# Kernel optimization log

Measured on AMD Instinct MI355X. Metric: run time of the kernel, lower is better.

Reference implementation:

```python
import jax, jax.numpy as jnp
import numpy as np

N, E, IN_DIM, H, OUT, MAPD = 20000, 640000, 24, 128, 24, 512
SLOPE = 0.01  # torch F.leaky_relu default


def setup_inputs() -> dict:
    key = jax.random.key(0)
    ks = jax.random.split(key, 20)
    g = lambda i, shape, s: jax.random.normal(ks[i], shape, jnp.float32) * s
    inp = {
        "feats": g(0, (N, IN_DIM), 1.0),
        "e_w": jax.random.uniform(ks[1], (E, 1), dtype=jnp.float32),
        "maps_embedding": g(2, (N, MAPD), 1.0),
        "snorm_n": jnp.ones((N, 1), jnp.float32),
        "src": jax.random.randint(ks[3], (E,), 0, N),
        "dst": jax.random.randint(ks[4], (E,), 0, N),
        "W_eh": g(5, (H, IN_DIM), (2.0 / IN_DIM) ** 0.5), "b_eh": jnp.zeros((H,), jnp.float32),
        "W_ee": g(6, (H, 1), 1.0), "b_ee": jnp.zeros((H,), jnp.float32),
        "W_cat": g(7, (H, H + MAPD), (2.0 / (H + MAPD)) ** 0.5), "b_cat": jnp.zeros((H,), jnp.float32),
        "Ws1": g(8, (H, H), (2.0 / H) ** 0.5), "Wf1": g(9, (H, H), (2.0 / H) ** 0.5),
        "a1": g(10, (2 * H,), (2.0 / (2 * H)) ** 0.5),
        "Ws2": g(11, (H, H), (2.0 / H) ** 0.5), "Wf2": g(12, (H, H), (2.0 / H) ** 0.5),
        "a2": g(13, (2 * H,), (2.0 / (2 * H)) ** 0.5),
        "W_out": g(14, (OUT, H), (2.0 / H) ** 0.5), "b_out": jnp.zeros((OUT,), jnp.float32),
    }
    return inp


def gat_layer(h, src, dst, Ws, Wf, a):
    # My_GATLayer with (as constructed in My_GAT) relu=False, att_ew=False, dropouts=0.
    h_in = h
    h_s = h @ Ws.T                         # [N,H] self transform
    z = h @ Wf.T                           # [N,H] message transform
    # attention score = leaky_relu(a^T [z_src, z_dst]) computed via per-node halves
    s_src = z @ a[:H]                      # [N]
    s_dst = z @ a[H:]                      # [N]
    e = jax.nn.leaky_relu(s_src[src] + s_dst[dst], SLOPE)          # [E]
    # numerically stable segment softmax over incoming edges grouped by dst
    m = jax.ops.segment_max(e, dst, num_segments=N)
    m = jnp.where(jnp.isfinite(m), m, 0.0)
    ex = jnp.exp(e - m[dst])
    denom = jax.ops.segment_sum(ex, dst, num_segments=N)
    alpha = ex / jnp.maximum(denom[dst], 1e-16)                    # [E]
    agg = jax.ops.segment_sum(alpha[:, None] * z[src], dst, num_segments=N)  # [N,H]
    indeg = jax.ops.segment_sum(jnp.ones_like(e), dst, num_segments=N)
    # DGL update_all leaves zero-in-degree nodes at their prior ndata['h'] (= h_in)
    h_node = jnp.where(indeg[:, None] > 0, h_s + agg, h_in)
    return h_in + h_node                   # residual connection; relu disabled (positional-arg bug)


def reference(feats, e_w, maps_embedding, snorm_n, src, dst,
              W_eh, b_eh, W_ee, b_ee, W_cat, b_cat,
              Ws1, Wf1, a1, Ws2, Wf2, a2, W_out, b_out):
    feats = feats.reshape(feats.shape[0], -1)
    h = feats @ W_eh.T + b_eh                                  # embedding_h
    _e = e_w @ W_ee.T + b_ee                                   # edge embedding (stored on g.edata['w'], unused since att_ew binds to attn_drop)
    h = jnp.concatenate([maps_embedding, h], axis=-1) @ W_cat.T + b_cat
    h = jax.nn.relu(h)
    h = gat_layer(h, src, dst, Ws1, Wf1, a1)
    h = gat_layer(h, src, dst, Ws2, Wf2, a2)
    return h @ W_out.T + b_out
```

## Files before the change

kernel.cpp:

```cpp
#include <hip/hip_runtime.h>

#define HBLK 128
#define EPB 4096

typedef __attribute__((ext_vector_type(8))) short s8v;
typedef __attribute__((ext_vector_type(4))) float f32x4;
typedef __attribute__((ext_vector_type(8))) _Float16 h8f;

__device__ inline void split2(float x, short& h, short& l) {
    unsigned hb = __float_as_uint(x) & 0xFFFF0000u;
    float hf = __uint_as_float(hb);
    float lf = x - hf;
    h = (short)(hb >> 16);
    l = (short)(__float_as_uint(lf) >> 16);
}

__device__ inline void split8(const float4& a0, const float4& a1, s8v& ah, s8v& al) {
    float vv[8];
    *(float4*)&vv[0] = a0;
    *(float4*)&vv[4] = a1;
#pragma unroll
    for (int e = 0; e < 8; ++e) {
        short hh, ll;
        split2(vv[e], hh, ll);
        ah[e] = hh;
        al[e] = ll;
    }
}


__global__ void bin_hist(const int* __restrict__ dst, int* __restrict__ histT,
                         int E, int NB1) {
    __shared__ int h[256];
    const int t = threadIdx.x, blk = blockIdx.x;
    h[t] = 0;
    __syncthreads();
    const int e0 = blk * EPB;
    const int e1 = min(E, e0 + EPB);
    for (int e = e0 + t; e < e1; e += 256)
        atomicAdd(&h[dst[e] >> 7], 1);
    __syncthreads();
    histT[t * NB1 + blk] = h[t];
}

__global__ void scan1(const int* __restrict__ counts, int* __restrict__ offs,
                      int* __restrict__ bsums, int n) {
    __shared__ int lds[256];
    const int t = threadIdx.x;
    const int i = blockIdx.x * 256 + t;
    const int v = (i < n) ? counts[i] : 0;
    lds[t] = v;
    __syncthreads();
    for (int off = 1; off < 256; off <<= 1) {
        int add = (t >= off) ? lds[t - off] : 0;
        __syncthreads();
        lds[t] += add;
        __syncthreads();
    }
    if (i < n) offs[i] = lds[t] - v;
    if (t == 255) bsums[blockIdx.x] = lds[255];
}

__global__ void scan2(int* __restrict__ bsums, int nb) {
    __shared__ int lds[256];
    const int t = threadIdx.x;
    const int v = (t < nb) ? bsums[t] : 0;
    lds[t] = v;
    __syncthreads();
    for (int off = 1; off < 256; off <<= 1) {
        int add = (t >= off) ? lds[t - off] : 0;
        __syncthreads();
        lds[t] += add;
        __syncthreads();
    }
    if (t < nb) bsums[t] = lds[t] - v;
}

__global__ void scan3g(int* __restrict__ data, const int* __restrict__ bsums, int n) {
    const int i = blockIdx.x * 256 + threadIdx.x;
    if (i < n) data[i] += bsums[blockIdx.x];
}

__global__ void bin_scatter(const int* __restrict__ src, const int* __restrict__ dst,
                            const int* __restrict__ histT, int2* __restrict__ ebuf,
                            int E, int NB1) {
    __shared__ int cur[256];
    const int t = threadIdx.x, blk = blockIdx.x;
    cur[t] = histT[t * NB1 + blk];
    __syncthreads();
    const int e0 = blk * EPB;
    const int e1 = min(E, e0 + EPB);
    for (int e = e0 + t; e < e1; e += 256) {
        const int d = dst[e];
        const int p = atomicAdd(&cur[d >> 7], 1);
        ebuf[p] = make_int2(src[e], d);
    }
}

__global__ void bucket_sort(const int2* __restrict__ ebuf, const int* __restrict__ histT,
                            int* __restrict__ offs, int* __restrict__ srcs,
                            int N, int E, int NB1) {
    __shared__ int cnt[256];
    __shared__ int cur[256];
    const int t = threadIdx.x, b = blockIdx.x;
    const int ebase = histT[b * NB1];
    const int eend = (b + 1 < 256) ? histT[(b + 1) * NB1] : E;
    cnt[t] = 0;
    __syncthreads();
    for (int e = ebase + t; e < eend; e += 256)
        atomicAdd(&cnt[ebuf[e].y & 127], 1);
    __syncthreads();
    const int own = cnt[t];
    for (int off = 1; off < 256; off <<= 1) {
        int add = (t >= off) ? cnt[t - off] : 0;
        __syncthreads();
        cnt[t] += add;
        __syncthreads();
    }
    const int excl = cnt[t] - own;
    cur[t] = ebase + excl;
    const int node = (b << 7) + t;
    if (t < 128 && node < N) offs[node] = ebase + excl;
    if (b == 0 && t == 0) offs[N] = E;
    __syncthreads();
    for (int e = ebase + t; e < eend; e += 256) {
        const int2 ed = ebuf[e];
        const int p = atomicAdd(&cur[ed.y & 127], 1);
        srcs[p] = ed.x;
    }
}

__global__ void make_wcomb(const float* __restrict__ Wcat, int ldw, int mapd,
                           const float* __restrict__ Weh, int indim,
                           const float* __restrict__ beh, const float* __restrict__ bcat,
                           float* __restrict__ Wcomb, float* __restrict__ bcomb) {
    const int i = blockIdx.x * 256 + threadIdx.x;
    const int total = HBLK * indim;
    if (i < total) {
        const int c = i / indim, k = i % indim;
        const float* wc = Wcat + (long)c * ldw + mapd;
        float s = 0.f;
        for (int j = 0; j < HBLK; ++j) s += wc[j] * Weh[j * indim + k];
        Wcomb[(long)c * indim + k] = s;
    } else if (i < total + HBLK) {
        const int c = i - total;
        const float* wc = Wcat + (long)c * ldw + mapd;
        float s = bcat[c];
        for (int j = 0; j < HBLK; ++j) s += wc[j] * beh[j];
        bcomb[c] = s;
    }
}

__global__ void split_w_pack(const float* __restrict__ W, int ldw, int kin, int cin,
                             short* __restrict__ dh, short* __restrict__ dl,
                             int C, int K) {
    long i = (long)blockIdx.x * 256 + threadIdx.x;
    if (i >= (long)C * K) return;
    int c = (int)(i / K), k = (int)(i % K);
    float x = (k < kin && c < cin) ? W[(long)c * ldw + k] : 0.f;
    short h, l;
    split2(x, h, l);
    int nj = C >> 4;
    int j = c >> 4, l16 = c & 15;
    int chunk = k >> 5, quad = (k >> 3) & 3, t = k & 7;
    long off = (((long)(chunk * nj + j) * 64) + quad * 16 + l16) * 8 + t;
    dh[off] = h;
    dl[off] = l;
}

__global__ void pack_wcat(const float* __restrict__ Wcat, int ldw, int mapd,
                          const float* __restrict__ Wcomb, int indim,
                          short* __restrict__ dh, short* __restrict__ dl, int K) {
    long i = (long)blockIdx.x * 256 + threadIdx.x;
    if (i >= (long)HBLK * K) return;
    int c = (int)(i / K), k = (int)(i % K);
    float x = 0.f;
    if (k < mapd) x = Wcat[(long)c * ldw + k];
    else if (k < mapd + indim) x = Wcomb[(long)c * indim + (k - mapd)];
    short h, l;
    split2(x, h, l);
    int j = c >> 4, l16 = c & 15;
    int chunk = k >> 5, quad = (k >> 3) & 3, t = k & 7;
    long off = (((long)(chunk * 8 + j) * 64) + quad * 16 + l16) * 8 + t;
    dh[off] = h;
    dl[off] = l;
}

__global__ void split_w_pack4(const float* __restrict__ W0, const float* __restrict__ W1,
                              const float* __restrict__ W2, const float* __restrict__ W3,
                              short* __restrict__ dh, short* __restrict__ dl) {
    const float* Ws[4] = {W0, W1, W2, W3};
    const int m = blockIdx.y;
    long i = (long)blockIdx.x * 256 + threadIdx.x;
    int c = (int)(i >> 7), k = (int)(i & 127);
    float x = Ws[m][c * HBLK + k];
    short h, l;
    split2(x, h, l);
    int j = c >> 4, l16 = c & 15;
    int chunk = k >> 5, quad = (k >> 3) & 3, t = k & 7;
    long off = (long)m * 16384 + (((long)(chunk * 8 + j) * 64) + quad * 16 + l16) * 8 + t;
    dh[off] = h;
    dl[off] = l;
}

__global__ __launch_bounds__(256, 2) void gemm_bigk(
    const float* __restrict__ A1, int lda1, int K1,
    const float* __restrict__ A2, int lda2, int Kin,
    int K,
    const short* __restrict__ Wh, const short* __restrict__ Wl,
    const float* __restrict__ bias,
    float* __restrict__ Cf, int M)
{
    __shared__ short lds_h[2][4096];
    __shared__ short lds_l[2][4096];
    const int tid = threadIdx.x;
    const int wv = tid >> 6;
    const int lane = tid & 63;
    const int l16 = lane & 15;
    const int quad = lane >> 4;
    const int m0 = blockIdx.x * 64 + wv * 16;
    int ra = m0 + l16;
    if (ra >= M) ra = M - 1;
    const long r1 = (long)ra * lda1;
    const long r2 = (long)ra * lda2;
    const int NC = K >> 5;

    f32x4 acc[8];
#pragma unroll
    for (int j = 0; j < 8; ++j) acc[j] = (f32x4){0.f, 0.f, 0.f, 0.f};

#define LOAD_A(d0, d1, kb)                                      \
    {                                                           \
        const int col0 = (kb) + quad * 8;                       \
        if (col0 < K1) {                                        \
            const float* ap = A1 + r1 + col0;                   \
            d0 = *(const float4*)ap;                            \
            d1 = *(const float4*)(ap + 4);                      \
        } else if (col0 < Kin) {                                \
            const float* ap = A2 + r2 + (col0 - K1);            \
            d0 = *(const float4*)ap;                            \
            d1 = *(const float4*)(ap + 4);                      \
        } else {                                                \
            d0 = make_float4(0.f, 0.f, 0.f, 0.f);               \
            d1 = make_float4(0.f, 0.f, 0.f, 0.f);               \
        }                                                       \
    }
#define LOAD_W(c)                                               \
    {                                                           \
        const int4* gh = (const int4*)(Wh + (long)(c) * 4096);  \
        const int4* gl = (const int4*)(Wl + (long)(c) * 4096);  \
        wh0 = gh[tid * 2]; wh1 = gh[tid * 2 + 1];               \
        wl0 = gl[tid * 2]; wl1 = gl[tid * 2 + 1];               \
    }
#define WRITE_W(b)                                              \
    {                                                           \
        int4* bh = (int4*)lds_h[b];                             \
        int4* bl = (int4*)lds_l[b];                             \
        bh[tid * 2] = wh0; bh[tid * 2 + 1] = wh1;               \
        bl[tid * 2] = wl0; bl[tid * 2 + 1] = wl1;               \
    }

    int4 wh0, wh1, wl0, wl1;
    LOAD_W(0)
    WRITE_W(0)
    LOAD_W(1)
    float4 a0c, a1c, a0n, a1n;
    float4 a0p = make_float4(0.f, 0.f, 0.f, 0.f);
    float4 a1p = make_float4(0.f, 0.f, 0.f, 0.f);
    LOAD_A(a0c, a1c, 0)
    LOAD_A(a0n, a1n, 32)
    asm volatile("s_waitcnt lgkmcnt(0)" ::: "memory");
    __builtin_amdgcn_s_barrier();
    asm volatile("" ::: "memory");

    for (int c = 0; c < NC; ++c) {
        const int nb = c & 1;
        if (c + 2 < NC) {
            LOAD_A(a0p, a1p, (c + 2) * 32)
        }
        s8v ah, al;
        split8(a0c, a1c, ah, al);
#pragma unroll
        for (int j = 0; j < 8; ++j) {
            const s8v whf = *(const s8v*)&lds_h[nb][(j * 64 + lane) * 8];
            const s8v wlf = *(const s8v*)&lds_l[nb][(j * 64 + lane) * 8];
            acc[j] = __builtin_amdgcn_mfma_f32_16x16x32_bf16(ah, whf, acc[j], 0, 0, 0);
            acc[j] = __builtin_amdgcn_mfma_f32_16x16x32_bf16(ah, wlf, acc[j], 0, 0, 0);
            acc[j] = __builtin_amdgcn_mfma_f32_16x16x32_bf16(al, whf, acc[j], 0, 0, 0);
        }
        if (c + 1 < NC) {
            WRITE_W(nb ^ 1)
            if (c + 2 < NC) LOAD_W(c + 2)
            asm volatile("s_waitcnt lgkmcnt(0)" ::: "memory");
            __builtin_amdgcn_s_barrier();
            asm volatile("" ::: "memory");
        }
        a0c = a0n; a1c = a1n; a0n = a0p; a1n = a1p;
    }
#undef LOAD_A
#undef LOAD_W
#undef WRITE_W

#pragma unroll
    for (int r = 0; r < 4; ++r) {
        const int gr = m0 + quad * 4 + r;
        if (gr >= M) continue;
#pragma unroll
        for (int j = 0; j < 8; ++j) {
            const int col = j * 16 + l16;
            float v = acc[j][r] + bias[col];
            Cf[(long)gr * HBLK + col] = fmaxf(v, 0.f);
        }
    }
}

__global__ __launch_bounds__(256, 2) void gemm_smallk(
    const float* __restrict__ A,
    const short* __restrict__ W1h, const short* __restrict__ W1l,
    const short* __restrict__ W2h, const short* __restrict__ W2l,
    float* __restrict__ C1f, _Float16* __restrict__ Czh,
    const float* __restrict__ avec,
    float* __restrict__ sOut, float* __restrict__ dOut, int M)
{
    __shared__ short lh[16384];
    __shared__ short ll[16384];
    const short* __restrict__ Wh = blockIdx.y ? W2h : W1h;
    const short* __restrict__ Wl = blockIdx.y ? W2l : W1l;
    float* __restrict__ Cf = blockIdx.y ? nullptr : C1f;
    _Float16* __restrict__ Ch16 = blockIdx.y ? Czh : nullptr;
    const float* __restrict__ av = blockIdx.y ? avec : nullptr;
    const int tid = threadIdx.x;
    const int wv = tid >> 6;
    const int lane = tid & 63;
    const int l16 = lane & 15;
    const int quad = lane >> 4;
    const int m0 = blockIdx.x * 64 + wv * 16;
    int ra = m0 + l16;
    if (ra >= M) ra = M - 1;
    const float* arow = A + (long)ra * HBLK + quad * 8;

    {
        const int4* gh = (const int4*)Wh;
        const int4* gl = (const int4*)Wl;
        int4* bh = (int4*)lh;
        int4* bl = (int4*)ll;
#pragma unroll
        for (int i = 0; i < 8; ++i) {
            bh[i * 256 + tid] = gh[i * 256 + tid];
            bl[i * 256 + tid] = gl[i * 256 + tid];
        }
    }
    float4 aw0[4], aw1[4];
#pragma unroll
    for (int c = 0; c < 4; ++c) {
        aw0[c] = *(const float4*)(arow + c * 32);
        aw1[c] = *(const float4*)(arow + c * 32 + 4);
    }
    f32x4 acc[8];
#pragma unroll
    for (int j = 0; j < 8; ++j) acc[j] = (f32x4){0.f, 0.f, 0.f, 0.f};
    __syncthreads();

#pragma unroll
    for (int c = 0; c < 4; ++c) {
        s8v ah, al;
        split8(aw0[c], aw1[c], ah, al);
#pragma unroll
        for (int j = 0; j < 8; ++j) {
            const s8v whf = *(const s8v*)&lh[((c * 8 + j) * 64 + lane) * 8];
            const s8v wlf = *(const s8v*)&ll[((c * 8 + j) * 64 + lane) * 8];
            acc[j] = __builtin_amdgcn_mfma_f32_16x16x32_bf16(ah, whf, acc[j], 0, 0, 0);
            acc[j] = __builtin_amdgcn_mfma_f32_16x16x32_bf16(ah, wlf, acc[j], 0, 0, 0);
            acc[j] = __builtin_amdgcn_mfma_f32_16x16x32_bf16(al, whf, acc[j], 0, 0, 0);
        }
    }

#pragma unroll
    for (int r = 0; r < 4; ++r) {
        const int gr = m0 + quad * 4 + r;
        if (gr >= M) continue;
#pragma unroll
        for (int j = 0; j < 8; ++j) {
            const int col = j * 16 + l16;
            const float v = acc[j][r];
            if (Cf) Cf[(long)gr * HBLK + col] = v;
            if (Ch16) Ch16[(long)gr * HBLK + col] = (_Float16)v;
        }
    }

    if (av) {
        float av0[8], av1[8];
#pragma unroll
        for (int j = 0; j < 8; ++j) {
            av0[j] = av[j * 16 + l16];
            av1[j] = av[128 + j * 16 + l16];
        }
#pragma unroll
        for (int r = 0; r < 4; ++r) {
            float ssp = 0.f, sdp = 0.f;
#pragma unroll
            for (int j = 0; j < 8; ++j) {
                const float v = acc[j][r];
                ssp += v * av0[j];
                sdp += v * av1[j];
            }
#pragma unroll
            for (int off = 1; off < 16; off <<= 1) {
                ssp += __shfl_xor(ssp, off);
                sdp += __shfl_xor(sdp, off);
            }
            const int gr = m0 + quad * 4 + r;
            if (l16 == 0 && gr < M) {
                sOut[gr] = ssp;
                dOut[gr] = sdp;
            }
        }
    }
}

__global__ __launch_bounds__(256) void gemm_out(
    const float* __restrict__ A,
    const short* __restrict__ Wh, const short* __restrict__ Wl,
    const float* __restrict__ bias, float* __restrict__ out,
    int M, int OUTD)
{
    __shared__ short lh[4096], ll[4096];
    const int tid = threadIdx.x;
    {
        const int4* gh = (const int4*)Wh;
        const int4* gl = (const int4*)Wl;
        int4* bh = (int4*)lh;
        int4* bl = (int4*)ll;
        bh[tid * 2] = gh[tid * 2];
        bh[tid * 2 + 1] = gh[tid * 2 + 1];
        bl[tid * 2] = gl[tid * 2];
        bl[tid * 2 + 1] = gl[tid * 2 + 1];
    }
    const int wv = tid >> 6;
    const int lane = tid & 63;
    const int l16 = lane & 15;
    const int quad = lane >> 4;
    const int m0 = blockIdx.x * 64 + wv * 16;
    int ra = m0 + l16;
    if (ra >= M) ra = M - 1;
    const float* arow = A + (long)ra * HBLK + quad * 8;

    f32x4 acc[2];
    acc[0] = (f32x4){0.f, 0.f, 0.f, 0.f};
    acc[1] = (f32x4){0.f, 0.f, 0.f, 0.f};
    __syncthreads();

#pragma unroll
    for (int c = 0; c < 4; ++c) {
        const float4 a0 = *(const float4*)(arow + c * 32);
        const float4 a1 = *(const float4*)(arow + c * 32 + 4);
        s8v ah, al;
        split8(a0, a1, ah, al);
#pragma unroll
        for (int j = 0; j < 2; ++j) {
            const s8v whf = *(const s8v*)&lh[((c * 2 + j) * 64 + lane) * 8];
            const s8v wlf = *(const s8v*)&ll[((c * 2 + j) * 64 + lane) * 8];
            acc[j] = __builtin_amdgcn_mfma_f32_16x16x32_bf16(ah, whf, acc[j], 0, 0, 0);
            acc[j] = __builtin_amdgcn_mfma_f32_16x16x32_bf16(ah, wlf, acc[j], 0, 0, 0);
            acc[j] = __builtin_amdgcn_mfma_f32_16x16x32_bf16(al, whf, acc[j], 0, 0, 0);
        }
    }

#pragma unroll
    for (int r = 0; r < 4; ++r) {
        const int gr = m0 + quad * 4 + r;
        if (gr >= M) continue;
#pragma unroll
        for (int j = 0; j < 2; ++j) {
            const int col = j * 16 + l16;
            if (col < OUTD)
                out[(long)gr * OUTD + col] = acc[j][r] + bias[col];
        }
    }
}

__global__ void gat_gather(const float* __restrict__ h_in, const float* __restrict__ hs,
                           const _Float16* __restrict__ zh,
                           const float* __restrict__ s_src, const float* __restrict__ s_dst,
                           const int* __restrict__ offs, const int* __restrict__ srcs,
                           float* __restrict__ h_out, int N) {
    const int wave = threadIdx.x >> 6;
    const int lane = threadIdx.x & 63;
    const int n = blockIdx.x * 4 + wave;
    if (n >= N) return;
    const int g = lane >> 4, l = lane & 15;
    const int beg = offs[n], end = offs[n + 1];

    float acc[8] = {};
    if (end > beg) {
        const float sd = s_dst[n];
        float m = -INFINITY, s = 0.f;
        for (int i = beg + lane; i < end; i += 64) {
            float e = sd + s_src[srcs[i]];
            e = e > 0.f ? e : 0.01f * e;
            float nm = fmaxf(m, e);
            s = s * __expf(m - nm) + __expf(e - nm);
            m = nm;
        }
#pragma unroll
        for (int off = 32; off > 0; off >>= 1) {
            float m2 = __shfl_down(m, off);
            float s2 = __shfl_down(s, off);
            if (m2 > m) {
                float t = m; m = m2; m2 = t;
                float ts = s; s = s2; s2 = ts;
            }
            s = (m == -INFINITY) ? 0.f : s + s2 * __expf(m2 - m);
        }
        m = __shfl(m, 0);
        s = __shfl(s, 0);
        const float inv = 1.f / fmaxf(s, 1e-16f);

        int i = beg + g;
        for (; i + 4 < end; i += 8) {
            const int s0 = srcs[i];
            const int s1 = srcs[i + 4];
            float e0 = sd + s_src[s0];
            float e1 = sd + s_src[s1];
            e0 = e0 > 0.f ? e0 : 0.01f * e0;
            e1 = e1 > 0.f ? e1 : 0.01f * e1;
            const float w0 = __expf(e0 - m) * inv;
            const float w1 = __expf(e1 - m) * inv;
            const h8f z0 = *(const h8f*)(zh + (long)s0 * HBLK + 8 * l);
            const h8f z1 = *(const h8f*)(zh + (long)s1 * HBLK + 8 * l);
#pragma unroll
            for (int e = 0; e < 8; ++e)
                acc[e] += w0 * (float)z0[e] + w1 * (float)z1[e];
        }
        if (i < end) {
            const int s0 = srcs[i];
            float e0 = sd + s_src[s0];
            e0 = e0 > 0.f ? e0 : 0.01f * e0;
            const float w0 = __expf(e0 - m) * inv;
            const h8f z0 = *(const h8f*)(zh + (long)s0 * HBLK + 8 * l);
#pragma unroll
            for (int e = 0; e < 8; ++e)
                acc[e] += w0 * (float)z0[e];
        }
#pragma unroll
        for (int e = 0; e < 8; ++e) {
            acc[e] += __shfl_down(acc[e], 32);
            acc[e] += __shfl_down(acc[e], 16);
        }
    }

    if (g == 0) {
        const long base = (long)n * HBLK + 8 * l;
        const float4 hi0 = *(const float4*)(h_in + base);
        const float4 hi1 = *(const float4*)(h_in + base + 4);
        float o[8];
        if (end > beg) {
            const float4 hv0 = *(const float4*)(hs + base);
            const float4 hv1 = *(const float4*)(hs + base + 4);
            const float* hip = (const float*)&hi0;
            const float* hvp = (const float*)&hv0;
#pragma unroll
            for (int e = 0; e < 4; ++e) o[e] = hip[e] + hvp[e] + acc[e];
            const float* hip1 = (const float*)&hi1;
            const float* hvp1 = (const float*)&hv1;
#pragma unroll
            for (int e = 0; e < 4; ++e) o[4 + e] = hip1[e] + hvp1[e] + acc[4 + e];
        } else {
            const float* hip = (const float*)&hi0;
            const float* hip1 = (const float*)&hi1;
#pragma unroll
            for (int e = 0; e < 4; ++e) o[e] = 2.f * hip[e];
#pragma unroll
            for (int e = 0; e < 4; ++e) o[4 + e] = 2.f * hip1[e];
        }
        *(float4*)(h_out + base) = *(float4*)&o[0];
        *(float4*)(h_out + base + 4) = *(float4*)&o[4];
    }
}

extern "C" void kernel_launch(void* const* d_in, const int* in_sizes, int n_in,
                              void* d_out, int out_size, void* d_ws, size_t ws_size,
                              hipStream_t stream) {
    const float* feats = (const float*)d_in[0];
    const float* maps  = (const float*)d_in[2];
    const int* src = (const int*)d_in[4];
    const int* dst = (const int*)d_in[5];
    const float* W_eh  = (const float*)d_in[6];
    const float* b_eh  = (const float*)d_in[7];
    const float* W_cat = (const float*)d_in[10];
    const float* b_cat = (const float*)d_in[11];
    const float* Ws1 = (const float*)d_in[12];
    const float* Wf1 = (const float*)d_in[13];
    const float* a1  = (const float*)d_in[14];
    const float* Ws2 = (const float*)d_in[15];
    const float* Wf2 = (const float*)d_in[16];
    const float* a2  = (const float*)d_in[17];
    const float* W_out = (const float*)d_in[18];
    const float* b_out = (const float*)d_in[19];

    const int N = in_sizes[3];
    const int E = in_sizes[4];
    const int IN_DIM = in_sizes[0] / N;
    const int MAPD = in_sizes[2] / N;
    const int OUTD = in_sizes[19];
    const int KCAT = MAPD + HBLK;
    const int KC = (MAPD + IN_DIM + 31) & ~31;

    char* p = (char*)d_ws;
    const size_t NH = (size_t)N * HBLK;
    float* hin  = (float*)p;  p += NH * 4;
    float* hs   = (float*)p;  p += NH * 4;
    float* hout = (float*)p;  p += NH * 4;
    _Float16* zh = (_Float16*)p; p += NH * 2;
    float* ssrc = (float*)p;  p += (size_t)N * 4;
    float* sdst = (float*)p;  p += (size_t)N * 4;
    int* offs   = (int*)p;    p += (size_t)(N + 1) * 4;
    int* srcs   = (int*)p;    p += (size_t)E * 4;
    int* bsums  = (int*)p;    p += 256 * 4;
    int* histT  = (int*)p;    p += (size_t)256 * 256 * 4;
    float* Wcomb = (float*)p; p += (size_t)HBLK * IN_DIM * 4;
    float* bcomb = (float*)p; p += (size_t)HBLK * 4;
    p = (char*)(((uintptr_t)p + 15) & ~(uintptr_t)15);
    int2* ebuf = (int2*)p;    p += (size_t)E * 8;
    short* Wcat_h = (short*)p; p += (size_t)HBLK * KC * 2;
    short* Wcat_l = (short*)p; p += (size_t)HBLK * KC * 2;
    short* Wout_h = (short*)p; p += (size_t)32 * HBLK * 2;
    short* Wout_l = (short*)p; p += (size_t)32 * HBLK * 2;
    short* Wly_h = (short*)p;  p += (size_t)4 * HBLK * HBLK * 2;
    short* Wly_l = (short*)p;  p += (size_t)4 * HBLK * HBLK * 2;

    const int NB1 = (E + EPB - 1) / EPB;
    const int NBUCK = (N + 127) >> 7;
    const int nHist = 256 * NB1;
    bin_hist<<<NB1, 256, 0, stream>>>(dst, histT, E, NB1);
    scan1<<<NB1, 256, 0, stream>>>(histT, histT, bsums, nHist);
    scan2<<<1, 256, 0, stream>>>(bsums, NB1);
    scan3g<<<NB1, 256, 0, stream>>>(histT, bsums, nHist);
    bin_scatter<<<NB1, 256, 0, stream>>>(src, dst, histT, ebuf, E, NB1);
    bucket_sort<<<NBUCK, 256, 0, stream>>>(ebuf, histT, offs, srcs, N, E, NB1);

    make_wcomb<<<(HBLK * IN_DIM + HBLK + 255) / 256, 256, 0, stream>>>(
        W_cat, KCAT, MAPD, W_eh, IN_DIM, b_eh, b_cat, Wcomb, bcomb);
    pack_wcat<<<(HBLK * KC + 255) / 256, 256, 0, stream>>>(
        W_cat, KCAT, MAPD, Wcomb, IN_DIM, Wcat_h, Wcat_l, KC);
    split_w_pack4<<<dim3(64, 4), 256, 0, stream>>>(Ws1, Wf1, Ws2, Wf2, Wly_h, Wly_l);
    split_w_pack<<<(32 * HBLK + 255) / 256, 256, 0, stream>>>(
        W_out, HBLK, HBLK, OUTD, Wout_h, Wout_l, 32, HBLK);

    const int gGrid = (N + 63) / 64;
    const int n4 = (N + 3) / 4;

    gemm_bigk<<<gGrid, 256, 0, stream>>>(
        maps, MAPD, MAPD, feats, IN_DIM, MAPD + IN_DIM, KC,
        Wcat_h, Wcat_l, bcomb, hin, N);

    gemm_smallk<<<dim3(gGrid, 2), 256, 0, stream>>>(
        hin, Wly_h, Wly_l, Wly_h + 16384, Wly_l + 16384,
        hs, zh, a1, ssrc, sdst, N);
    gat_gather<<<n4, 256, 0, stream>>>(hin, hs, zh, ssrc, sdst, offs, srcs, hout, N);

    gemm_smallk<<<dim3(gGrid, 2), 256, 0, stream>>>(
        hout, Wly_h + 32768, Wly_l + 32768, Wly_h + 49152, Wly_l + 49152,
        hs, zh, a2, ssrc, sdst, N);
    gat_gather<<<n4, 256, 0, stream>>>(hout, hs, zh, ssrc, sdst, offs, srcs, hin, N);

    gemm_out<<<gGrid, 256, 0, stream>>>(hin, Wout_h, Wout_l, b_out, (float*)d_out, N, OUTD);
}
```

Baseline: 274.1 us.

## Fold scan fixup and weight packing into fewer launches, deepen prefetch and unroll gather

Removes the scan3g kernel by adding block sums inline in bin_scatter and bucket_sort. Merges make_wcomb into pack_wcat and folds the W_out packing into split_w_packA, cutting three launches in total. Separately, gemm_bigk now prefetches weights and A one chunk further ahead, and the GAT gather loop processes four edges per iteration instead of two. The deeper prefetch and wider unroll raise register pressure, and each pack_wcat thread does a 128-long dot product for the combined columns.

```diff
diff --git a/kernel.cpp b/kernel.cpp
--- a/kernel.cpp
+++ b/kernel.cpp
@@ -76,17 +76,13 @@
     if (t < nb) bsums[t] = lds[t] - v;
 }
 
-__global__ void scan3g(int* __restrict__ data, const int* __restrict__ bsums, int n) {
-    const int i = blockIdx.x * 256 + threadIdx.x;
-    if (i < n) data[i] += bsums[blockIdx.x];
-}
-
 __global__ void bin_scatter(const int* __restrict__ src, const int* __restrict__ dst,
-                            const int* __restrict__ histT, int2* __restrict__ ebuf,
-                            int E, int NB1) {
+                            const int* __restrict__ histT, const int* __restrict__ bsums,
+                            int2* __restrict__ ebuf, int E, int NB1) {
     __shared__ int cur[256];
     const int t = threadIdx.x, blk = blockIdx.x;
-    cur[t] = histT[t * NB1 + blk];
+    const int li = t * NB1 + blk;
+    cur[t] = histT[li] + bsums[li >> 8];
     __syncthreads();
     const int e0 = blk * EPB;
     const int e1 = min(E, e0 + EPB);
@@ -98,13 +94,19 @@
 }
 
 __global__ void bucket_sort(const int2* __restrict__ ebuf, const int* __restrict__ histT,
+                            const int* __restrict__ bsums,
                             int* __restrict__ offs, int* __restrict__ srcs,
                             int N, int E, int NB1) {
     __shared__ int cnt[256];
     __shared__ int cur[256];
     const int t = threadIdx.x, b = blockIdx.x;
-    const int ebase = histT[b * NB1];
-    const int eend = (b + 1 < 256) ? histT[(b + 1) * NB1] : E;
+    const int li0 = b * NB1;
+    const int ebase = histT[li0] + bsums[li0 >> 8];
+    int eend = E;
+    if (b + 1 < 256) {
+        const int li1 = (b + 1) * NB1;
+        eend = histT[li1] + bsums[li1 >> 8];
+    }
     cnt[t] = 0;
     __syncthreads();
     for (int e = ebase + t; e < eend; e += 256)
@@ -130,20 +132,34 @@
     }
 }
 
-__global__ void make_wcomb(const float* __restrict__ Wcat, int ldw, int mapd,
-                           const float* __restrict__ Weh, int indim,
-                           const float* __restrict__ beh, const float* __restrict__ bcat,
-                           float* __restrict__ Wcomb, float* __restrict__ bcomb) {
-    const int i = blockIdx.x * 256 + threadIdx.x;
-    const int total = HBLK * indim;
+__global__ void pack_wcat(const float* __restrict__ Wcat, int ldw, int mapd,
+                          const float* __restrict__ Weh, int indim,
+                          const float* __restrict__ beh, const float* __restrict__ bcat,
+                          short* __restrict__ dh, short* __restrict__ dl,
+                          float* __restrict__ bcomb, int K) {
+    const long i = (long)blockIdx.x * 256 + threadIdx.x;
+    const long total = (long)HBLK * K;
     if (i < total) {
-        const int c = i / indim, k = i % indim;
-        const float* wc = Wcat + (long)c * ldw + mapd;
-        float s = 0.f;
-        for (int j = 0; j < HBLK; ++j) s += wc[j] * Weh[j * indim + k];
-        Wcomb[(long)c * indim + k] = s;
+        const int c = (int)(i / K), k = (int)(i % K);
+        float x = 0.f;
+        if (k < mapd) {
+            x = Wcat[(long)c * ldw + k];
+        } else if (k < mapd + indim) {
+            const float* wc = Wcat + (long)c * ldw + mapd;
+            const int kk = k - mapd;
+            float s = 0.f;
+            for (int j = 0; j < HBLK; ++j) s += wc[j] * Weh[j * indim + kk];
+            x = s;
+        }
+        short h, l;
+        split2(x, h, l);
+        const int j = c >> 4, l16 = c & 15;
+        const int chunk = k >> 5, quad = (k >> 3) & 3, t = k & 7;
+        const long off = (((long)(chunk * 8 + j) * 64) + quad * 16 + l16) * 8 + t;
+        dh[off] = h;
+        dl[off] = l;
     } else if (i < total + HBLK) {
-        const int c = i - total;
+        const int c = (int)(i - total);
         const float* wc = Wcat + (long)c * ldw + mapd;
         float s = bcat[c];
         for (int j = 0; j < HBLK; ++j) s += wc[j] * beh[j];
@@ -151,56 +167,36 @@
     }
 }
 
-__global__ void split_w_pack(const float* __restrict__ W, int ldw, int kin, int cin,
-                             short* __restrict__ dh, short* __restrict__ dl,
-                             int C, int K) {
-    long i = (long)blockIdx.x * 256 + threadIdx.x;
-    if (i >= (long)C * K) return;
-    int c = (int)(i / K), k = (int)(i % K);
-    float x = (k < kin && c < cin) ? W[(long)c * ldw + k] : 0.f;
-    short h, l;
-    split2(x, h, l);
-    int nj = C >> 4;
-    int j = c >> 4, l16 = c & 15;
-    int chunk = k >> 5, quad = (k >> 3) & 3, t = k & 7;
-    long off = (((long)(chunk * nj + j) * 64) + quad * 16 + l16) * 8 + t;
-    dh[off] = h;
-    dl[off] = l;
-}
-
-__global__ void pack_wcat(const float* __restrict__ Wcat, int ldw, int mapd,
-                          const float* __restrict__ Wcomb, int indim,
-                          short* __restrict__ dh, short* __restrict__ dl, int K) {
-    long i = (long)blockIdx.x * 256 + threadIdx.x;
-    if (i >= (long)HBLK * K) return;
-    int c = (int)(i / K), k = (int)(i % K);
-    float x = 0.f;
-    if (k < mapd) x = Wcat[(long)c * ldw + k];
-    else if (k < mapd + indim) x = Wcomb[(long)c * indim + (k - mapd)];
-    short h, l;
-    split2(x, h, l);
-    int j = c >> 4, l16 = c & 15;
-    int chunk = k >> 5, quad = (k >> 3) & 3, t = k & 7;
-    long off = (((long)(chunk * 8 + j) * 64) + quad * 16 + l16) * 8 + t;
-    dh[off] = h;
-    dl[off] = l;
-}
-
-__global__ void split_w_pack4(const float* __restrict__ W0, const float* __restrict__ W1,
+__global__ void split_w_packA(const float* __restrict__ W0, const float* __restrict__ W1,
                               const float* __restrict__ W2, const float* __restrict__ W3,
-                              short* __restrict__ dh, short* __restrict__ dl) {
-    const float* Ws[4] = {W0, W1, W2, W3};
+                              const float* __restrict__ Wout, int outd,
+                              short* __restrict__ dh, short* __restrict__ dl,
+                              short* __restrict__ doh, short* __restrict__ dol) {
     const int m = blockIdx.y;
-    long i = (long)blockIdx.x * 256 + threadIdx.x;
-    int c = (int)(i >> 7), k = (int)(i & 127);
-    float x = Ws[m][c * HBLK + k];
-    short h, l;
-    split2(x, h, l);
-    int j = c >> 4, l16 = c & 15;
-    int chunk = k >> 5, quad = (k >> 3) & 3, t = k & 7;
-    long off = (long)m * 16384 + (((long)(chunk * 8 + j) * 64) + quad * 16 + l16) * 8 + t;
-    dh[off] = h;
-    dl[off] = l;
+    const long i = (long)blockIdx.x * 256 + threadIdx.x;
+    if (m < 4) {
+        const float* Ws[4] = {W0, W1, W2, W3};
+        const int c = (int)(i >> 7), k = (int)(i & 127);
+        float x = Ws[m][c * HBLK + k];
+        short h, l;
+        split2(x, h, l);
+        const int j = c >> 4, l16 = c & 15;
+        const int chunk = k >> 5, quad = (k >> 3) & 3, t = k & 7;
+        const long off = (long)m * 16384 + (((long)(chunk * 8 + j) * 64) + quad * 16 + l16) * 8 + t;
+        dh[off] = h;
+        dl[off] = l;
+    } else {
+        if (i >= 32 * HBLK) return;
+        const int c = (int)(i >> 7), k = (int)(i & 127);
+        float x = (c < outd) ? Wout[c * HBLK + k] : 0.f;
+        short h, l;
+        split2(x, h, l);
+        const int j = c >> 4, l16 = c & 15;
+        const int chunk = k >> 5, quad = (k >> 3) & 3, t = k & 7;
+        const long off = (((long)(chunk * 2 + j) * 64) + quad * 16 + l16) * 8 + t;
+        doh[off] = h;
+        dol[off] = l;
+    }
 }
 
 __global__ __launch_bounds__(256, 2) void gemm_bigk(
@@ -245,38 +241,40 @@
             d1 = make_float4(0.f, 0.f, 0.f, 0.f);               \
         }                                                       \
     }
-#define LOAD_W(c)                                               \
+#define LOAD_W(r0, r1w, r2w, r3, c)                             \
     {                                                           \
         const int4* gh = (const int4*)(Wh + (long)(c) * 4096);  \
         const int4* gl = (const int4*)(Wl + (long)(c) * 4096);  \
-        wh0 = gh[tid * 2]; wh1 = gh[tid * 2 + 1];               \
-        wl0 = gl[tid * 2]; wl1 = gl[tid * 2 + 1];               \
-    }
-#define WRITE_W(b)                                              \
+        r0 = gh[tid * 2]; r1w = gh[tid * 2 + 1];                \
+        r2w = gl[tid * 2]; r3 = gl[tid * 2 + 1];                \
+    }
+#define WRITE_W(b, r0, r1w, r2w, r3)                            \
     {                                                           \
         int4* bh = (int4*)lds_h[b];                             \
         int4* bl = (int4*)lds_l[b];                             \
-        bh[tid * 2] = wh0; bh[tid * 2 + 1] = wh1;               \
-        bl[tid * 2] = wl0; bl[tid * 2 + 1] = wl1;               \
-    }
-
-    int4 wh0, wh1, wl0, wl1;
-    LOAD_W(0)
-    WRITE_W(0)
-    LOAD_W(1)
-    float4 a0c, a1c, a0n, a1n;
-    float4 a0p = make_float4(0.f, 0.f, 0.f, 0.f);
-    float4 a1p = make_float4(0.f, 0.f, 0.f, 0.f);
+        bh[tid * 2] = r0; bh[tid * 2 + 1] = r1w;                \
+        bl[tid * 2] = r2w; bl[tid * 2 + 1] = r3;                \
+    }
+
+    int4 wa0, wa1, wa2, wa3, wb0, wb1, wb2, wb3;
+    LOAD_W(wa0, wa1, wa2, wa3, 0)
+    WRITE_W(0, wa0, wa1, wa2, wa3)
+    LOAD_W(wa0, wa1, wa2, wa3, 1)
+    LOAD_W(wb0, wb1, wb2, wb3, 2)
+    float4 a0c, a1c, a0n, a1n, a0p, a1p;
+    float4 a0q = make_float4(0.f, 0.f, 0.f, 0.f);
+    float4 a1q = make_float4(0.f, 0.f, 0.f, 0.f);
     LOAD_A(a0c, a1c, 0)
     LOAD_A(a0n, a1n, 32)
+    LOAD_A(a0p, a1p, 64)
     asm volatile("s_waitcnt lgkmcnt(0)" ::: "memory");
     __builtin_amdgcn_s_barrier();
     asm volatile("" ::: "memory");
 
     for (int c = 0; c < NC; ++c) {
         const int nb = c & 1;
-        if (c + 2 < NC) {
-            LOAD_A(a0p, a1p, (c + 2) * 32)
+        if (c + 3 < NC) {
+            LOAD_A(a0q, a1q, (c + 3) * 32)
         }
         s8v ah, al;
         split8(a0c, a1c, ah, al);
@@ -289,13 +287,16 @@
             acc[j] = __builtin_amdgcn_mfma_f32_16x16x32_bf16(al, whf, acc[j], 0, 0, 0);
         }
         if (c + 1 < NC) {
-            WRITE_W(nb ^ 1)
-            if (c + 2 < NC) LOAD_W(c + 2)
+            WRITE_W(nb ^ 1, wa0, wa1, wa2, wa3)
+            wa0 = wb0; wa1 = wb1; wa2 = wb2; wa3 = wb3;
+            if (c + 3 < NC) LOAD_W(wb0, wb1, wb2, wb3, c + 3)
             asm volatile("s_waitcnt lgkmcnt(0)" ::: "memory");
             __builtin_amdgcn_s_barrier();
             asm volatile("" ::: "memory");
         }
-        a0c = a0n; a1c = a1n; a0n = a0p; a1n = a1p;
+        a0c = a0n; a1c = a1n;
+        a0n = a0p; a1n = a1p;
+        a0p = a0q; a1p = a1q;
     }
 #undef LOAD_A
 #undef LOAD_W
@@ -517,22 +518,33 @@
         const float inv = 1.f / fmaxf(s, 1e-16f);
 
         int i = beg + g;
-        for (; i + 4 < end; i += 8) {
+        for (; i + 12 < end; i += 16) {
             const int s0 = srcs[i];
             const int s1 = srcs[i + 4];
+            const int s2i = srcs[i + 8];
+            const int s3 = srcs[i + 12];
             float e0 = sd + s_src[s0];
             float e1 = sd + s_src[s1];
+            float e2 = sd + s_src[s2i];
+            float e3 = sd + s_src[s3];
             e0 = e0 > 0.f ? e0 : 0.01f * e0;
             e1 = e1 > 0.f ? e1 : 0.01f * e1;
+            e2 = e2 > 0.f ? e2 : 0.01f * e2;
+            e3 = e3 > 0.f ? e3 : 0.01f * e3;
             const float w0 = __expf(e0 - m) * inv;
             const float w1 = __expf(e1 - m) * inv;
+            const float w2 = __expf(e2 - m) * inv;
+            const float w3 = __expf(e3 - m) * inv;
             const h8f z0 = *(const h8f*)(zh + (long)s0 * HBLK + 8 * l);
             const h8f z1 = *(const h8f*)(zh + (long)s1 * HBLK + 8 * l);
+            const h8f z2 = *(const h8f*)(zh + (long)s2i * HBLK + 8 * l);
+            const h8f z3 = *(const h8f*)(zh + (long)s3 * HBLK + 8 * l);
 #pragma unroll
             for (int e = 0; e < 8; ++e)
-                acc[e] += w0 * (float)z0[e] + w1 * (float)z1[e];
-        }
-        if (i < end) {
+                acc[e] += w0 * (float)z0[e] + w1 * (float)z1[e]
+                        + w2 * (float)z2[e] + w3 * (float)z3[e];
+        }
+        for (; i < end; i += 4) {
             const int s0 = srcs[i];
             float e0 = sd + s_src[s0];
             e0 = e0 > 0.f ? e0 : 0.01f * e0;
@@ -618,7 +630,6 @@
     int* srcs   = (int*)p;    p += (size_t)E * 4;
     int* bsums  = (int*)p;    p += 256 * 4;
     int* histT  = (int*)p;    p += (size_t)256 * 256 * 4;
-    float* Wcomb = (float*)p; p += (size_t)HBLK * IN_DIM * 4;
     float* bcomb = (float*)p; p += (size_t)HBLK * 4;
     p = (char*)(((uintptr_t)p + 15) & ~(uintptr_t)15);
     int2* ebuf = (int2*)p;    p += (size_t)E * 8;
@@ -635,17 +646,13 @@
     bin_hist<<<NB1, 256, 0, stream>>>(dst, histT, E, NB1);
     scan1<<<NB1, 256, 0, stream>>>(histT, histT, bsums, nHist);
     scan2<<<1, 256, 0, stream>>>(bsums, NB1);
-    scan3g<<<NB1, 256, 0, stream>>>(histT, bsums, nHist);
-    bin_scatter<<<NB1, 256, 0, stream>>>(src, dst, histT, ebuf, E, NB1);
-    bucket_sort<<<NBUCK, 256, 0, stream>>>(ebuf, histT, offs, srcs, N, E, NB1);
-
-    make_wcomb<<<(HBLK * IN_DIM + HBLK + 255) / 256, 256, 0, stream>>>(
-        W_cat, KCAT, MAPD, W_eh, IN_DIM, b_eh, b_cat, Wcomb, bcomb);
-    pack_wcat<<<(HBLK * KC + 255) / 256, 256, 0, stream>>>(
-        W_cat, KCAT, MAPD, Wcomb, IN_DIM, Wcat_h, Wcat_l, KC);
-    split_w_pack4<<<dim3(64, 4), 256, 0, stream>>>(Ws1, Wf1, Ws2, Wf2, Wly_h, Wly_l);
-    split_w_pack<<<(32 * HBLK + 255) / 256, 256, 0, stream>>>(
-        W_out, HBLK, HBLK, OUTD, Wout_h, Wout_l, 32, HBLK);
+    bin_scatter<<<NB1, 256, 0, stream>>>(src, dst, histT, bsums, ebuf, E, NB1);
+    bucket_sort<<<NBUCK, 256, 0, stream>>>(ebuf, histT, bsums, offs, srcs, N, E, NB1);
+
+    pack_wcat<<<(HBLK * KC + HBLK + 255) / 256, 256, 0, stream>>>(
+        W_cat, KCAT, MAPD, W_eh, IN_DIM, b_eh, b_cat, Wcat_h, Wcat_l, bcomb, KC);
+    split_w_packA<<<dim3(64, 5), 256, 0, stream>>>(
+        Ws1, Wf1, Ws2, Wf2, W_out, OUTD, Wly_h, Wly_l, Wout_h, Wout_l);
 
     const int gGrid = (N + 63) / 64;
     const int n4 = (N + 3) / 4;
```

Measured after the change: 270.3 us. Within noise of the previous version (-1.4%).
